# Optimization experiments

Hardware: AMD Instinct MI355X
Metric: run time of the kernel (lower is better)

Reference implementation:

```python
import jax, jax.numpy as jnp
import numpy as np

B, S, H = 1, 2048, 1024
NQ, NKV, HD = 16, 8, 64
FF, E, TOPK = 2048, 4, 2
WINDOW = 512
CAP = 50.0
CLIP_L, CLIP_R = -0.03, 1.03
EPS = 1e-5
ROPE_BASE = 10000.0


def setup_inputs() -> dict:
    key = jax.random.key(0)
    ks = jax.random.split(key, 14)
    std = 0.02
    def nrm(k, shape):
        return jax.random.normal(k, shape, jnp.float32) * std
    return {
        'x': jax.random.normal(ks[0], (B, S, H), jnp.float32),
        'norm1_w': 1.0 + nrm(ks[1], (H,)),
        'wq': nrm(ks[2], (H, NQ * HD)),
        'wk': nrm(ks[3], (H, NKV * HD)),
        'wv': nrm(ks[4], (H, NKV * HD)),
        'wo': nrm(ks[5], (NQ * HD, H)),
        'qn_w': 1.0 + nrm(ks[6], (HD,)),
        'kn_w': 1.0 + nrm(ks[7], (HD,)),
        'norm2_w': 1.0 + nrm(ks[8], (H,)),
        'gate_w': nrm(ks[9], (H, E)),
        'w_gate': nrm(ks[10], (E, H, FF)),
        'w_up': nrm(ks[11], (E, H, FF)),
        'w_down': nrm(ks[12], (E, FF, H)),
    }


def _rms(x, w):
    return x * jax.lax.rsqrt(jnp.mean(x * x, axis=-1, keepdims=True) + EPS) * w


def _rope(t):
    # t: [B, S, N, D]
    D = t.shape[-1]
    half = D // 2
    inv = 1.0 / (ROPE_BASE ** (jnp.arange(half, dtype=jnp.float32) / half))
    ang = jnp.arange(t.shape[1], dtype=jnp.float32)[:, None] * inv  # [S, half]
    cos = jnp.cos(ang)[None, :, None, :]
    sin = jnp.sin(ang)[None, :, None, :]
    t1, t2 = t[..., :half], t[..., half:]
    return jnp.concatenate([t1 * cos - t2 * sin, t1 * sin + t2 * cos], axis=-1)


def reference(x, norm1_w, wq, wk, wv, wo, qn_w, kn_w, norm2_w, gate_w, w_gate, w_up, w_down):
    # --- self-attention block ---
    xn = _rms(x, norm1_w)
    q = (xn @ wq).reshape(B, S, NQ, HD)
    k = (xn @ wk).reshape(B, S, NKV, HD)
    v = (xn @ wv).reshape(B, S, NKV, HD)
    q = _rms(_rope(q), qn_w)  # RoPE then QK-norm over head_dim
    k = _rms(_rope(k), kn_w)
    rep = NQ // NKV
    k = jnp.repeat(k, rep, axis=2)  # GQA expand to NQ heads
    v = jnp.repeat(v, rep, axis=2)
    scale = 1.0 / np.sqrt(HD).astype(np.float32)
    scores = jnp.einsum('bqhd,bkhd->bhqk', q, k) * scale
    scores = CAP * jnp.tanh(scores / CAP)  # softmax capping (overrides temperature)
    i = jnp.arange(S)[:, None]
    j = jnp.arange(S)[None, :]
    allow = (j <= i) & (i - j < WINDOW)  # causal + sliding window
    scores = jnp.where(allow[None, None], scores, -jnp.inf)
    p = jax.nn.softmax(scores, axis=-1)
    p = jnp.clip((CLIP_R - CLIP_L) * p + CLIP_L, 0.0, 1.0)  # softmax clipping
    attn = jnp.einsum('bhqk,bkhd->bqhd', p, v).reshape(B, S, NQ * HD)
    h = x + attn @ wo
    # --- MoE gated-SiLU MLP block ---
    xn2 = _rms(h, norm2_w).reshape(B * S, H)
    probs = jax.nn.softmax(xn2 @ gate_w, axis=-1)
    topv, topi = jax.lax.top_k(probs, TOPK)
    topv = topv / jnp.sum(topv, axis=-1, keepdims=True)
    T = B * S
    wdense = jnp.zeros((T, E), jnp.float32).at[jnp.arange(T)[:, None], topi].add(topv)
    g = jnp.einsum('th,ehf->etf', xn2, w_gate)
    u = jnp.einsum('th,ehf->etf', xn2, w_up)
    y = jnp.einsum('etf,efh->eth', jax.nn.silu(g) * u, w_down)
    moe = jnp.einsum('eth,te->th', y, wdense)
    return h + moe.reshape(B, S, H)
```

## Files before the change

kernel.cpp:

```cpp
#include <hip/hip_runtime.h>
#include <hip/hip_bf16.h>
#include <math.h>

#define S_LEN   2048
#define H_DIM   1024
#define N_QH    16
#define N_KVH   8
#define HEADD   64
#define FF_DIM  2048
#define N_EXP   4
#define WIN     512
#define QB      16

typedef __attribute__((ext_vector_type(8))) short bf16x8;
typedef __attribute__((ext_vector_type(4))) float f32x4;

__device__ __forceinline__ short f2bf(float x) {
  unsigned u = __float_as_uint(x);
  u += 0x7fffu + ((u >> 16) & 1u);
  return (short)(u >> 16);
}
__device__ __forceinline__ float bf2f(short h) {
  return __uint_as_float((unsigned)(unsigned short)h << 16);
}
__device__ __forceinline__ int swz(int row, int col) {
  return row * 64 + (col ^ ((row & 7) << 3));
}

__global__ __launch_bounds__(256) void k_rope_tables(float* __restrict__ ct, float* __restrict__ st) {
  int i = blockIdx.x * 256 + threadIdx.x;
  int t = i >> 5, d = i & 31;
  double inv = 1.0 / pow(10000.0, (double)d / 32.0);
  double ang = (double)t * inv;
  ct[i] = (float)cos(ang);
  st[i] = (float)sin(ang);
}

template <int MODE>
__global__ __launch_bounds__(256) void k_rmsnorm(const float* __restrict__ x,
                                                 const float* __restrict__ w,
                                                 short* __restrict__ yh,
                                                 short* __restrict__ yl,
                                                 const float* __restrict__ gw,
                                                 float* __restrict__ wd) {
  int row = blockIdx.x;
  const float4 v = ((const float4*)(x + (long)row * H_DIM))[threadIdx.x];
  float ss = v.x * v.x + v.y * v.y + v.z * v.z + v.w * v.w;
  for (int off = 32; off; off >>= 1) ss += __shfl_xor(ss, off);
  __shared__ float red[4];
  if ((threadIdx.x & 63) == 0) red[threadIdx.x >> 6] = ss;
  __syncthreads();
  ss = red[0] + red[1] + red[2] + red[3];
  float r = (float)(1.0 / sqrt((double)ss * (1.0 / 1024.0) + 1e-5));
  const float4 wv = ((const float4*)w)[threadIdx.x];
  float4 o;
  o.x = v.x * r * wv.x; o.y = v.y * r * wv.y; o.z = v.z * r * wv.z; o.w = v.w * r * wv.w;
  if (MODE == 2) {
    short h0 = f2bf(o.x), h1 = f2bf(o.y), h2 = f2bf(o.z), h3 = f2bf(o.w);
    short l0 = f2bf(o.x - bf2f(h0)), l1 = f2bf(o.y - bf2f(h1));
    short l2 = f2bf(o.z - bf2f(h2)), l3 = f2bf(o.w - bf2f(h3));
    uint2 hv = make_uint2((unsigned short)h0 | ((unsigned)(unsigned short)h1 << 16),
                          (unsigned short)h2 | ((unsigned)(unsigned short)h3 << 16));
    uint2 lv = make_uint2((unsigned short)l0 | ((unsigned)(unsigned short)l1 << 16),
                          (unsigned short)l2 | ((unsigned)(unsigned short)l3 << 16));
    ((uint2*)(yh + (long)row * H_DIM))[threadIdx.x] = hv;
    ((uint2*)(yl + (long)row * H_DIM))[threadIdx.x] = lv;
  }
  if (MODE == 3) {
    unsigned lo = (unsigned short)f2bf(o.x) | ((unsigned)(unsigned short)f2bf(o.y) << 16);
    unsigned hi = (unsigned short)f2bf(o.z) | ((unsigned)(unsigned short)f2bf(o.w) << 16);
    ((uint2*)(yh + (long)row * H_DIM))[threadIdx.x] = make_uint2(lo, hi);
    int i0 = threadIdx.x * 4;
    float4 g0 = *(const float4*)&gw[(i0 + 0) * 4];
    float4 g1 = *(const float4*)&gw[(i0 + 1) * 4];
    float4 g2 = *(const float4*)&gw[(i0 + 2) * 4];
    float4 g3 = *(const float4*)&gw[(i0 + 3) * 4];
    float p0 = o.x * g0.x + o.y * g1.x + o.z * g2.x + o.w * g3.x;
    float p1 = o.x * g0.y + o.y * g1.y + o.z * g2.y + o.w * g3.y;
    float p2 = o.x * g0.z + o.y * g1.z + o.z * g2.z + o.w * g3.z;
    float p3 = o.x * g0.w + o.y * g1.w + o.z * g2.w + o.w * g3.w;
    for (int off = 32; off; off >>= 1) {
      p0 += __shfl_xor(p0, off); p1 += __shfl_xor(p1, off);
      p2 += __shfl_xor(p2, off); p3 += __shfl_xor(p3, off);
    }
    __shared__ float gred[4][4];
    int wid = threadIdx.x >> 6;
    if ((threadIdx.x & 63) == 0) { gred[wid][0] = p0; gred[wid][1] = p1; gred[wid][2] = p2; gred[wid][3] = p3; }
    __syncthreads();
    if (threadIdx.x == 0) {
      float l[4];
      for (int e = 0; e < 4; ++e) l[e] = gred[0][e] + gred[1][e] + gred[2][e] + gred[3][e];
      int i1 = 0;
      for (int e = 1; e < 4; ++e) if (l[e] > l[i1]) i1 = e;
      int i2 = -1;
      for (int e = 0; e < 4; ++e) { if (e == i1) continue; if (i2 < 0 || l[e] > l[i2]) i2 = e; }
      float e2 = expf(l[i2] - l[i1]);
      float w1 = 1.f / (1.f + e2);
      float ov[4] = {0.f, 0.f, 0.f, 0.f};
      ov[i1] = w1; ov[i2] = 1.f - w1;
      wd[row * 4 + 0] = ov[0]; wd[row * 4 + 1] = ov[1];
      wd[row * 4 + 2] = ov[2]; wd[row * 4 + 3] = ov[3];
    }
  }
}

__global__ __launch_bounds__(256) void k_tsplit(const float* __restrict__ in,
                                                short* __restrict__ oh,
                                                short* __restrict__ ol, int R, int C) {
  __shared__ float tile[32][33];
  int bx = blockIdx.x, by = blockIdx.y;
  int lx = threadIdx.x & 31, ly = threadIdx.x >> 5;
  int xc = bx * 32 + lx;
#pragma unroll
  for (int k = 0; k < 4; ++k) {
    int y = by * 32 + ly + k * 8;
    tile[ly + k * 8][lx] = in[(long)y * C + xc];
  }
  __syncthreads();
  int ox = by * 32 + lx;
#pragma unroll
  for (int k = 0; k < 4; ++k) {
    int oy = bx * 32 + ly + k * 8;
    float v = tile[lx][ly + k * 8];
    short hb = f2bf(v);
    short lb = f2bf(v - bf2f(hb));
    oh[(long)oy * R + ox] = hb;
    ol[(long)oy * R + ox] = lb;
  }
}

__global__ __launch_bounds__(256) void k_transpose_cast(const float* __restrict__ in,
                                                        short* __restrict__ out,
                                                        int R, int C) {
  __shared__ float tile[32][33];
  int bx = blockIdx.x, by = blockIdx.y;
  int lx = threadIdx.x & 31, ly = threadIdx.x >> 5;
  int x = bx * 32 + lx;
#pragma unroll
  for (int k = 0; k < 4; ++k) {
    int y = by * 32 + ly + k * 8;
    tile[ly + k * 8][lx] = in[(long)y * C + x];
  }
  __syncthreads();
  int ox = by * 32 + lx;
#pragma unroll
  for (int k = 0; k < 4; ++k) {
    int oy = bx * 32 + ly + k * 8;
    out[(long)oy * R + ox] = f2bf(tile[lx][ly + k * 8]);
  }
}

template <int ADD>
__global__ __launch_bounds__(256) void k_gemm_split(const short* __restrict__ Ah,
                                                    const short* __restrict__ Al,
                                                    const short* __restrict__ Bh,
                                                    const short* __restrict__ Bl,
                                                    const float* __restrict__ R,
                                                    float* __restrict__ C,
                                                    int K, int ldA, int ldB, int ldC) {
  __shared__ short AsH[128 * 64], AsL[128 * 64], BsH[128 * 64], BsL[128 * 64];
  const int r0 = blockIdx.x * 128, c0 = blockIdx.y * 128;
  const int tid = threadIdx.x;
  const int wid = tid >> 6, lane = tid & 63;
  const int wr = wid >> 1, wc = wid & 1;
  const int lr = lane & 15, lg = lane >> 4;
  f32x4 zero = {0.f, 0.f, 0.f, 0.f};
  f32x4 acc[4][4];
#pragma unroll
  for (int m = 0; m < 4; ++m)
#pragma unroll
    for (int n = 0; n < 4; ++n) acc[m][n] = zero;
  for (int k0 = 0; k0 < K; k0 += 64) {
#pragma unroll
    for (int it = 0; it < 4; ++it) {
      int flat = tid + it * 256;
      int row = flat >> 3, cb = (flat & 7) * 8;
      int d = swz(row, cb);
      *(uint4*)&AsH[d] = *(const uint4*)&Ah[(long)(r0 + row) * ldA + k0 + cb];
      *(uint4*)&AsL[d] = *(const uint4*)&Al[(long)(r0 + row) * ldA + k0 + cb];
      *(uint4*)&BsH[d] = *(const uint4*)&Bh[(long)(c0 + row) * ldB + k0 + cb];
      *(uint4*)&BsL[d] = *(const uint4*)&Bl[(long)(c0 + row) * ldB + k0 + cb];
    }
    __syncthreads();
#pragma unroll
    for (int kk = 0; kk < 64; kk += 32) {
      bf16x8 ah[4], al[4], bh[4], bl[4];
#pragma unroll
      for (int m = 0; m < 4; ++m) {
        int d = swz(wr * 64 + m * 16 + lr, kk + lg * 8);
        ah[m] = *(const bf16x8*)&AsH[d];
        al[m] = *(const bf16x8*)&AsL[d];
      }
#pragma unroll
      for (int n = 0; n < 4; ++n) {
        int d = swz(wc * 64 + n * 16 + lr, kk + lg * 8);
        bh[n] = *(const bf16x8*)&BsH[d];
        bl[n] = *(const bf16x8*)&BsL[d];
      }
#pragma unroll
      for (int m = 0; m < 4; ++m)
#pragma unroll
        for (int n = 0; n < 4; ++n) {
          acc[m][n] = __builtin_amdgcn_mfma_f32_16x16x32_bf16(ah[m], bh[n], acc[m][n], 0, 0, 0);
          acc[m][n] = __builtin_amdgcn_mfma_f32_16x16x32_bf16(ah[m], bl[n], acc[m][n], 0, 0, 0);
          acc[m][n] = __builtin_amdgcn_mfma_f32_16x16x32_bf16(al[m], bh[n], acc[m][n], 0, 0, 0);
        }
    }
    __syncthreads();
  }
#pragma unroll
  for (int m = 0; m < 4; ++m)
#pragma unroll
    for (int n = 0; n < 4; ++n) {
      int col = c0 + wc * 64 + n * 16 + lr;
#pragma unroll
      for (int r = 0; r < 4; ++r) {
        int row = r0 + wr * 64 + m * 16 + lg * 4 + r;
        float v = acc[m][n][r];
        if (ADD) v += R[(long)row * ldC + col];
        C[(long)row * ldC + col] = v;
      }
    }
}

__global__ __launch_bounds__(256) void k_rope_rms(float* __restrict__ qkv,
                                                  const float* __restrict__ qn_w,
                                                  const float* __restrict__ kn_w,
                                                  const float* __restrict__ ct,
                                                  const float* __restrict__ st) {
  int idx = blockIdx.x * 4 + (threadIdx.x >> 6);
  int lane = threadIdx.x & 63;
  int t = idx / 24, hh = idx - t * 24;
  long base; const float* w;
  if (hh < N_QH) { base = (long)t * 2048 + hh * HEADD;              w = qn_w; }
  else           { base = (long)t * 2048 + 1024 + (hh - N_QH) * HEADD; w = kn_w; }
  float x = qkv[base + lane];
  float partner = __shfl_xor(x, 32);
  int d = lane & 31;
  float cs = ct[t * 32 + d], sn = st[t * 32 + d];
  float r = x * cs + partner * ((lane < 32) ? -sn : sn);
  float ss = r * r;
  for (int off = 32; off; off >>= 1) ss += __shfl_xor(ss, off);
  float rr = (float)(1.0 / sqrt((double)ss * (1.0 / 64.0) + 1e-5));
  qkv[base + lane] = r * rr * w[lane];
}

__global__ __launch_bounds__(256) void k_attn_mfma(const float* __restrict__ qkv,
                                                   short* __restrict__ attHi,
                                                   short* __restrict__ attLo) {
  __shared__ short Kh[64][72], Kl[64][72];
  __shared__ float sc[QB][580];
  __shared__ float row_a[QB];
  const int i0 = blockIdx.x * QB;
  const int hq = blockIdx.y;
  const int kvh = hq >> 1;
  const int tid = threadIdx.x;
  const int wv = tid >> 6, lane = tid & 63;
  const int lr = lane & 15, lg = lane >> 4;
  const int jstart = max(0, i0 - (WIN - 1));
  const int nch = (i0 + QB - jstart + 63) >> 6;
  const int ncols = nch * 64;
  f32x4 zero = {0.f, 0.f, 0.f, 0.f};

  bf16x8 qh[2], ql[2];
  {
    const float* qp = &qkv[(long)(i0 + lr) * 2048 + hq * HEADD];
#pragma unroll
    for (int kk = 0; kk < 2; ++kk) {
      float4 f0 = *(const float4*)&qp[kk * 32 + lg * 8];
      float4 f1 = *(const float4*)&qp[kk * 32 + lg * 8 + 4];
      float ff[8] = {f0.x, f0.y, f0.z, f0.w, f1.x, f1.y, f1.z, f1.w};
      bf16x8 h, l;
#pragma unroll
      for (int u = 0; u < 8; ++u) {
        short hb = f2bf(ff[u]);
        h[u] = hb; l[u] = f2bf(ff[u] - bf2f(hb));
      }
      qh[kk] = h; ql[kk] = l;
    }
  }

  for (int ch = 0; ch < nch; ++ch) {
    int jb = jstart + ch * 64;
    {
      int key = tid >> 2, dbase = (tid & 3) * 16;
      int j = jb + key;
      const float* kp = &qkv[(long)j * 2048 + 1024 + kvh * HEADD];
#pragma unroll
      for (int q4 = 0; q4 < 4; ++q4) {
        int d = dbase + q4 * 4;
        float4 f = make_float4(0.f, 0.f, 0.f, 0.f);
        if (j < S_LEN) f = *(const float4*)&kp[d];
        short h0 = f2bf(f.x), h1 = f2bf(f.y), h2 = f2bf(f.z), h3 = f2bf(f.w);
        short l0 = f2bf(f.x - bf2f(h0)), l1 = f2bf(f.y - bf2f(h1));
        short l2 = f2bf(f.z - bf2f(h2)), l3 = f2bf(f.w - bf2f(h3));
        *(uint2*)&Kh[key][d] = make_uint2(
            (unsigned short)h0 | ((unsigned)(unsigned short)h1 << 16),
            (unsigned short)h2 | ((unsigned)(unsigned short)h3 << 16));
        *(uint2*)&Kl[key][d] = make_uint2(
            (unsigned short)l0 | ((unsigned)(unsigned short)l1 << 16),
            (unsigned short)l2 | ((unsigned)(unsigned short)l3 << 16));
      }
    }
    __syncthreads();
    f32x4 s = zero;
#pragma unroll
    for (int kk = 0; kk < 2; ++kk) {
      bf16x8 kh = *(const bf16x8*)&Kh[wv * 16 + lr][kk * 32 + lg * 8];
      bf16x8 kl = *(const bf16x8*)&Kl[wv * 16 + lr][kk * 32 + lg * 8];
      s = __builtin_amdgcn_mfma_f32_16x16x32_bf16(qh[kk], kh, s, 0, 0, 0);
      s = __builtin_amdgcn_mfma_f32_16x16x32_bf16(qh[kk], kl, s, 0, 0, 0);
      s = __builtin_amdgcn_mfma_f32_16x16x32_bf16(ql[kk], kh, s, 0, 0, 0);
    }
    int colbase = ch * 64 + wv * 16;
#pragma unroll
    for (int r = 0; r < 4; ++r) {
      int q = 4 * lg + r;
      int i = i0 + q;
      int j = jb + wv * 16 + lr;
      float v = s[r] * 0.125f;
      v = 50.f * tanhf(v * 0.02f);
      bool allow = (j <= i) && (i - j < WIN);
      sc[q][colbase + lr] = allow ? v : -1e30f;
    }
    __syncthreads();
  }

  for (int r = wv * 4; r < wv * 4 + 4; ++r) {
    float mx = -1e30f;
    for (int n = lane; n < ncols; n += 64) mx = fmaxf(mx, sc[r][n]);
    for (int off = 32; off; off >>= 1) mx = fmaxf(mx, __shfl_xor(mx, off));
    float sum = 0.f;
    for (int n = lane; n < ncols; n += 64) {
      float p = expf(sc[r][n] - mx);
      sc[r][n] = p; sum += p;
    }
    for (int off = 32; off; off >>= 1) sum += __shfl_xor(sum, off);
    if (lane == 0) row_a[r] = 1.06f / sum;
  }
  __syncthreads();

  {
    int q = tid >> 4;
    float a = row_a[q];
    for (int n = (tid & 15); n < ncols; n += 16) {
      float e = sc[q][n];
      float p = fminf(fmaxf(fmaf(a, e, -0.03f), 0.f), 1.f);
      short ph = f2bf(p);
      short pl = f2bf(p - bf2f(ph));
      *(unsigned*)&sc[q][n] =
          (unsigned)(unsigned short)ph | ((unsigned)(unsigned short)pl << 16);
    }
  }
  __syncthreads();

  f32x4 oacc = zero;
  for (int ch = 0; ch < nch; ++ch) {
    int jb = jstart + ch * 64;
    {
      int j = jb + (lane);
      int dbase = wv * 16;
      bool ok = (j < S_LEN);
      const float* vp = &qkv[(long)j * 2048 + 1536 + kvh * HEADD];
#pragma unroll
      for (int dd = 0; dd < 16; ++dd) {
        float f = ok ? vp[dbase + dd] : 0.f;
        short hb = f2bf(f);
        Kh[dbase + dd][lane] = hb;
        Kl[dbase + dd][lane] = f2bf(f - bf2f(hb));
      }
    }
    __syncthreads();
#pragma unroll
    for (int kk = 0; kk < 2; ++kk) {
      const unsigned* pp = (const unsigned*)&sc[lr][ch * 64 + kk * 32 + lg * 8];
      uint4 w0 = *(const uint4*)&pp[0];
      uint4 w1 = *(const uint4*)&pp[4];
      bf16x8 pa, pb;
      pa[0] = (short)w0.x; pb[0] = (short)(w0.x >> 16);
      pa[1] = (short)w0.y; pb[1] = (short)(w0.y >> 16);
      pa[2] = (short)w0.z; pb[2] = (short)(w0.z >> 16);
      pa[3] = (short)w0.w; pb[3] = (short)(w0.w >> 16);
      pa[4] = (short)w1.x; pb[4] = (short)(w1.x >> 16);
      pa[5] = (short)w1.y; pb[5] = (short)(w1.y >> 16);
      pa[6] = (short)w1.z; pb[6] = (short)(w1.z >> 16);
      pa[7] = (short)w1.w; pb[7] = (short)(w1.w >> 16);
      bf16x8 vh = *(const bf16x8*)&Kh[wv * 16 + lr][kk * 32 + lg * 8];
      bf16x8 vl = *(const bf16x8*)&Kl[wv * 16 + lr][kk * 32 + lg * 8];
      oacc = __builtin_amdgcn_mfma_f32_16x16x32_bf16(pa, vh, oacc, 0, 0, 0);
      oacc = __builtin_amdgcn_mfma_f32_16x16x32_bf16(pa, vl, oacc, 0, 0, 0);
      oacc = __builtin_amdgcn_mfma_f32_16x16x32_bf16(pb, vh, oacc, 0, 0, 0);
    }
    __syncthreads();
  }
#pragma unroll
  for (int r = 0; r < 4; ++r) {
    int q = 4 * lg + r;
    int d = wv * 16 + lr;
    long ob = (long)(i0 + q) * 1024 + hq * HEADD + d;
    float v = oacc[r];
    short hb = f2bf(v);
    attHi[ob] = hb;
    attLo[ob] = f2bf(v - bf2f(hb));
  }
}

template <int ATOMIC>
__global__ __launch_bounds__(256) void k_gemm_bf16(const short* __restrict__ A,
                                                   const short* __restrict__ Bt,
                                                   float* __restrict__ C,
                                                   int K, int ldA, int ldB, int ldC,
                                                   long sA, long sB, long sC) {
  __shared__ short As[128 * 64];
  __shared__ short Bs[128 * 64];
  const int e = blockIdx.z;
  A += (long)e * sA; Bt += (long)e * sB; C += (long)e * sC;
  const int r0 = blockIdx.x * 128, c0 = blockIdx.y * 128;
  const int tid = threadIdx.x;
  const int wid = tid >> 6, lane = tid & 63;
  const int wr = wid >> 1, wc = wid & 1;
  const int lr = lane & 15, lg = lane >> 4;
  f32x4 zero = {0.f, 0.f, 0.f, 0.f};
  f32x4 acc[4][4];
#pragma unroll
  for (int m = 0; m < 4; ++m)
#pragma unroll
    for (int n = 0; n < 4; ++n) acc[m][n] = zero;
  for (int k0 = 0; k0 < K; k0 += 64) {
#pragma unroll
    for (int it = 0; it < 4; ++it) {
      int flat = tid + it * 256;
      int row = flat >> 3, cb = (flat & 7) * 8;
      int d = swz(row, cb);
      *(uint4*)&As[d] = *(const uint4*)&A[(long)(r0 + row) * ldA + k0 + cb];
      *(uint4*)&Bs[d] = *(const uint4*)&Bt[(long)(c0 + row) * ldB + k0 + cb];
    }
    __syncthreads();
#pragma unroll
    for (int kk = 0; kk < 64; kk += 32) {
      bf16x8 af[4], bfr[4];
#pragma unroll
      for (int m = 0; m < 4; ++m) af[m] = *(const bf16x8*)&As[swz(wr * 64 + m * 16 + lr, kk + lg * 8)];
#pragma unroll
      for (int n = 0; n < 4; ++n) bfr[n] = *(const bf16x8*)&Bs[swz(wc * 64 + n * 16 + lr, kk + lg * 8)];
#pragma unroll
      for (int m = 0; m < 4; ++m)
#pragma unroll
        for (int n = 0; n < 4; ++n)
          acc[m][n] = __builtin_amdgcn_mfma_f32_16x16x32_bf16(af[m], bfr[n], acc[m][n], 0, 0, 0);
    }
    __syncthreads();
  }
#pragma unroll
  for (int m = 0; m < 4; ++m)
#pragma unroll
    for (int n = 0; n < 4; ++n) {
      int col = c0 + wc * 64 + n * 16 + lr;
#pragma unroll
      for (int r = 0; r < 4; ++r) {
        int row = r0 + wr * 64 + m * 16 + lg * 4 + r;
        float v = acc[m][n][r];
        if (ATOMIC) atomicAdd(&C[(long)row * ldC + col], v);
        else        C[(long)row * ldC + col] = v;
      }
    }
}

__global__ __launch_bounds__(256) void k_moe_act(const float* __restrict__ gu,
                                                 const float* __restrict__ wd,
                                                 short* __restrict__ aAll,
                                                 int e) {
  long i4 = (long)blockIdx.x * 256 + threadIdx.x;
  int t  = (int)(i4 >> 9);
  int f4 = (int)(i4 & 511);
  float wte = wd[t * 4 + e];
  float4 g = ((const float4*)gu)[(long)t * 1024 + f4];
  float4 u = ((const float4*)gu)[(long)t * 1024 + 512 + f4];
  float4 s;
  s.x = wte * u.x * g.x / (1.f + expf(-g.x));
  s.y = wte * u.y * g.y / (1.f + expf(-g.y));
  s.z = wte * u.z * g.z / (1.f + expf(-g.z));
  s.w = wte * u.w * g.w / (1.f + expf(-g.w));
  unsigned lo = (unsigned short)f2bf(s.x) | ((unsigned)(unsigned short)f2bf(s.y) << 16);
  unsigned hi = (unsigned short)f2bf(s.z) | ((unsigned)(unsigned short)f2bf(s.w) << 16);
  ((uint2*)(aAll + ((long)e << 22)))[i4] = make_uint2(lo, hi);
}

extern "C" void kernel_launch(void* const* d_in, const int* in_sizes, int n_in,
                              void* d_out, int out_size, void* d_ws, size_t ws_size,
                              hipStream_t stream) {
  const float* x       = (const float*)d_in[0];
  const float* norm1_w = (const float*)d_in[1];
  const float* wq      = (const float*)d_in[2];
  const float* wk      = (const float*)d_in[3];
  const float* wv      = (const float*)d_in[4];
  const float* wo      = (const float*)d_in[5];
  const float* qn_w    = (const float*)d_in[6];
  const float* kn_w    = (const float*)d_in[7];
  const float* norm2_w = (const float*)d_in[8];
  const float* gate_w  = (const float*)d_in[9];
  const float* w_gate  = (const float*)d_in[10];
  const float* w_up    = (const float*)d_in[11];
  const float* w_down  = (const float*)d_in[12];
  float* out = (float*)d_out;
  char* ws = (char*)d_ws;
  const unsigned long MB = 1ul << 20;

  float* ropeC = (float*)(ws + 0);
  float* ropeS = (float*)(ws + 256 * 1024);
  float* qkv   = (float*)(ws + 1 * MB);
  short* xnHi  = (short*)(ws + 17 * MB);
  short* xnLo  = (short*)(ws + 21 * MB);
  short* attHi = (short*)(ws + 25 * MB);
  short* attLo = (short*)(ws + 29 * MB);
  float* gu    = (float*)(ws + 1 * MB);
  short* qkvWh = (short*)(ws + 33 * MB);
  short* qkvWl = (short*)(ws + 37 * MB);
  short* woTh  = (short*)(ws + 41 * MB);
  short* woTl  = (short*)(ws + 43 * MB);
  float* h     = (float*)(ws + 45 * MB);
  short* guT   = (short*)(ws + 45 * MB);
  short* x2b   = (short*)(ws + 53 * MB);
  float* wd    = (float*)(ws + 57 * MB);
  short* dT    = (short*)(ws + 58 * MB);
  short* aAll  = (short*)(ws + 74 * MB);

  k_rope_tables<<<256, 256, 0, stream>>>(ropeC, ropeS);
  k_rmsnorm<2><<<S_LEN, 256, 0, stream>>>(x, norm1_w, xnHi, xnLo, nullptr, nullptr);
  k_tsplit<<<dim3(32, 32), 256, 0, stream>>>(wq, qkvWh, qkvWl, 1024, 1024);
  k_tsplit<<<dim3(16, 32), 256, 0, stream>>>(wk, qkvWh + 1024 * 1024, qkvWl + 1024 * 1024, 1024, 512);
  k_tsplit<<<dim3(16, 32), 256, 0, stream>>>(wv, qkvWh + 1536 * 1024, qkvWl + 1536 * 1024, 1024, 512);
  k_tsplit<<<dim3(32, 32), 256, 0, stream>>>(wo, woTh, woTl, 1024, 1024);
  k_gemm_split<0><<<dim3(16, 16), 256, 0, stream>>>(xnHi, xnLo, qkvWh, qkvWl, nullptr, qkv,
                                                    1024, 1024, 1024, 2048);
  k_rope_rms<<<(S_LEN * 24) / 4, 256, 0, stream>>>(qkv, qn_w, kn_w, ropeC, ropeS);
  k_attn_mfma<<<dim3(S_LEN / QB, N_QH), 256, 0, stream>>>(qkv, attHi, attLo);
  k_gemm_split<1><<<dim3(16, 8), 256, 0, stream>>>(attHi, attLo, woTh, woTl, x, h,
                                                   1024, 1024, 1024, 1024);
  k_rmsnorm<3><<<S_LEN, 256, 0, stream>>>(h, norm2_w, x2b, nullptr, gate_w, wd);
  hipMemcpyAsync(out, h, (size_t)S_LEN * H_DIM * sizeof(float), hipMemcpyDeviceToDevice, stream);
  for (int e = 0; e < N_EXP; ++e)
    k_transpose_cast<<<dim3(1024 / 32, 2048 / 32), 256, 0, stream>>>(
        w_down + (long)e * FF_DIM * H_DIM, dT + (long)e * H_DIM * FF_DIM, 2048, 1024);
  for (int e = 0; e < N_EXP; ++e) {
    k_transpose_cast<<<dim3(2048 / 32, 1024 / 32), 256, 0, stream>>>(
        w_gate + (long)e * H_DIM * FF_DIM, guT, 1024, 2048);
    k_transpose_cast<<<dim3(2048 / 32, 1024 / 32), 256, 0, stream>>>(
        w_up + (long)e * H_DIM * FF_DIM, guT + (long)FF_DIM * H_DIM, 1024, 2048);
    k_gemm_bf16<0><<<dim3(16, 32), 256, 0, stream>>>(x2b, guT, gu, 1024, 1024, 1024, 4096, 0, 0, 0);
    k_moe_act<<<4096, 256, 0, stream>>>(gu, wd, aAll, e);
  }
  k_gemm_bf16<1><<<dim3(16, 8, N_EXP), 256, 0, stream>>>(
      aAll, dT, out, 2048, 2048, 2048, 1024,
      (long)S_LEN * FF_DIM, (long)H_DIM * FF_DIM, 0);
}
```

Baseline: 719.6 us.

## Precompute split-bf16 K and transposed V once, read directly in attention

Adds a kernel that converts K to hi/lo bf16 and V to transposed hi/lo bf16 once per KV head. Previously every attention block redid this conversion per chunk through shared memory. The attention kernel now loads MFMA operands straight from global memory and drops the per-chunk barriers. It also aligns the window start to 64 keys. The cost is an extra launch, extra workspace traffic, and uncoalesced per-lane global loads in place of LDS reads.

```diff
diff --git a/kernel.cpp b/kernel.cpp
--- a/kernel.cpp
+++ b/kernel.cpp
@@ -11,6 +11,7 @@
 #define N_EXP   4
 #define WIN     512
 #define QB      16
+#define SCS     596
 
 typedef __attribute__((ext_vector_type(8))) short bf16x8;
 typedef __attribute__((ext_vector_type(4))) float f32x4;
@@ -22,6 +23,9 @@
 }
 __device__ __forceinline__ float bf2f(short h) {
   return __uint_as_float((unsigned)(unsigned short)h << 16);
+}
+__device__ __forceinline__ unsigned pk2(short a, short b) {
+  return (unsigned)(unsigned short)a | ((unsigned)(unsigned short)b << 16);
 }
 __device__ __forceinline__ int swz(int row, int col) {
   return row * 64 + (col ^ ((row & 7) << 3));
@@ -59,17 +63,12 @@
     short h0 = f2bf(o.x), h1 = f2bf(o.y), h2 = f2bf(o.z), h3 = f2bf(o.w);
     short l0 = f2bf(o.x - bf2f(h0)), l1 = f2bf(o.y - bf2f(h1));
     short l2 = f2bf(o.z - bf2f(h2)), l3 = f2bf(o.w - bf2f(h3));
-    uint2 hv = make_uint2((unsigned short)h0 | ((unsigned)(unsigned short)h1 << 16),
-                          (unsigned short)h2 | ((unsigned)(unsigned short)h3 << 16));
-    uint2 lv = make_uint2((unsigned short)l0 | ((unsigned)(unsigned short)l1 << 16),
-                          (unsigned short)l2 | ((unsigned)(unsigned short)l3 << 16));
-    ((uint2*)(yh + (long)row * H_DIM))[threadIdx.x] = hv;
-    ((uint2*)(yl + (long)row * H_DIM))[threadIdx.x] = lv;
+    ((uint2*)(yh + (long)row * H_DIM))[threadIdx.x] = make_uint2(pk2(h0, h1), pk2(h2, h3));
+    ((uint2*)(yl + (long)row * H_DIM))[threadIdx.x] = make_uint2(pk2(l0, l1), pk2(l2, l3));
   }
   if (MODE == 3) {
-    unsigned lo = (unsigned short)f2bf(o.x) | ((unsigned)(unsigned short)f2bf(o.y) << 16);
-    unsigned hi = (unsigned short)f2bf(o.z) | ((unsigned)(unsigned short)f2bf(o.w) << 16);
-    ((uint2*)(yh + (long)row * H_DIM))[threadIdx.x] = make_uint2(lo, hi);
+    ((uint2*)(yh + (long)row * H_DIM))[threadIdx.x] =
+        make_uint2(pk2(f2bf(o.x), f2bf(o.y)), pk2(f2bf(o.z), f2bf(o.w)));
     int i0 = threadIdx.x * 4;
     float4 g0 = *(const float4*)&gw[(i0 + 0) * 4];
     float4 g1 = *(const float4*)&gw[(i0 + 1) * 4];
@@ -245,11 +244,59 @@
   qkv[base + lane] = r * rr * w[lane];
 }
 
-__global__ __launch_bounds__(256) void k_attn_mfma(const float* __restrict__ qkv,
-                                                   short* __restrict__ attHi,
-                                                   short* __restrict__ attLo) {
-  __shared__ short Kh[64][72], Kl[64][72];
-  __shared__ float sc[QB][580];
+__global__ __launch_bounds__(256) void k_kv_split(const float* __restrict__ qkv,
+                                                  short* __restrict__ Kbh, short* __restrict__ Kbl,
+                                                  short* __restrict__ Vth, short* __restrict__ Vtl) {
+  const int kvh = blockIdx.y;
+  const int jb = blockIdx.x * 64;
+  const int tid = threadIdx.x;
+  {
+    int j = jb + (tid >> 2);
+    int dq = (tid & 3) * 16;
+    const float* kp = &qkv[(long)j * 2048 + 1024 + kvh * HEADD + dq];
+    long ob = ((long)kvh * S_LEN + j) * HEADD + dq;
+#pragma unroll
+    for (int u4 = 0; u4 < 4; ++u4) {
+      float4 f = *(const float4*)&kp[u4 * 4];
+      short h0 = f2bf(f.x), h1 = f2bf(f.y), h2 = f2bf(f.z), h3 = f2bf(f.w);
+      short l0 = f2bf(f.x - bf2f(h0)), l1 = f2bf(f.y - bf2f(h1));
+      short l2 = f2bf(f.z - bf2f(h2)), l3 = f2bf(f.w - bf2f(h3));
+      *(uint2*)&Kbh[ob + u4 * 4] = make_uint2(pk2(h0, h1), pk2(h2, h3));
+      *(uint2*)&Kbl[ob + u4 * 4] = make_uint2(pk2(l0, l1), pk2(l2, l3));
+    }
+  }
+  {
+    int d = tid & 63;
+    int j0 = jb + (tid >> 6) * 16;
+    short hb[16], lb[16];
+#pragma unroll
+    for (int u = 0; u < 16; ++u) {
+      float f = qkv[(long)(j0 + u) * 2048 + 1536 + kvh * HEADD + d];
+      hb[u] = f2bf(f);
+      lb[u] = f2bf(f - bf2f(hb[u]));
+    }
+    long ob = ((long)kvh * HEADD + d) * S_LEN + j0;
+#pragma unroll
+    for (int w = 0; w < 2; ++w) {
+      uint4 oh, ol;
+      oh.x = pk2(hb[w * 8 + 0], hb[w * 8 + 1]); oh.y = pk2(hb[w * 8 + 2], hb[w * 8 + 3]);
+      oh.z = pk2(hb[w * 8 + 4], hb[w * 8 + 5]); oh.w = pk2(hb[w * 8 + 6], hb[w * 8 + 7]);
+      ol.x = pk2(lb[w * 8 + 0], lb[w * 8 + 1]); ol.y = pk2(lb[w * 8 + 2], lb[w * 8 + 3]);
+      ol.z = pk2(lb[w * 8 + 4], lb[w * 8 + 5]); ol.w = pk2(lb[w * 8 + 6], lb[w * 8 + 7]);
+      *(uint4*)&Vth[ob + w * 8] = oh;
+      *(uint4*)&Vtl[ob + w * 8] = ol;
+    }
+  }
+}
+
+__global__ __launch_bounds__(256) void k_attn2(const float* __restrict__ qkv,
+                                               const short* __restrict__ Kbh,
+                                               const short* __restrict__ Kbl,
+                                               const short* __restrict__ Vth,
+                                               const short* __restrict__ Vtl,
+                                               short* __restrict__ attHi,
+                                               short* __restrict__ attLo) {
+  __shared__ float sc[QB][SCS];
   __shared__ float row_a[QB];
   const int i0 = blockIdx.x * QB;
   const int hq = blockIdx.y;
@@ -257,10 +304,14 @@
   const int tid = threadIdx.x;
   const int wv = tid >> 6, lane = tid & 63;
   const int lr = lane & 15, lg = lane >> 4;
-  const int jstart = max(0, i0 - (WIN - 1));
+  const int jstart = (i0 >= WIN) ? ((i0 - (WIN - 1)) & ~63) : 0;
   const int nch = (i0 + QB - jstart + 63) >> 6;
   const int ncols = nch * 64;
   f32x4 zero = {0.f, 0.f, 0.f, 0.f};
+  const short* Kh_p = Kbh + (long)kvh * S_LEN * HEADD;
+  const short* Kl_p = Kbl + (long)kvh * S_LEN * HEADD;
+  const short* Vh_p = Vth + (long)kvh * HEADD * S_LEN;
+  const short* Vl_p = Vtl + (long)kvh * HEADD * S_LEN;
 
   bf16x8 qh[2], ql[2];
   {
@@ -282,49 +333,29 @@
 
   for (int ch = 0; ch < nch; ++ch) {
     int jb = jstart + ch * 64;
-    {
-      int key = tid >> 2, dbase = (tid & 3) * 16;
-      int j = jb + key;
-      const float* kp = &qkv[(long)j * 2048 + 1024 + kvh * HEADD];
-#pragma unroll
-      for (int q4 = 0; q4 < 4; ++q4) {
-        int d = dbase + q4 * 4;
-        float4 f = make_float4(0.f, 0.f, 0.f, 0.f);
-        if (j < S_LEN) f = *(const float4*)&kp[d];
-        short h0 = f2bf(f.x), h1 = f2bf(f.y), h2 = f2bf(f.z), h3 = f2bf(f.w);
-        short l0 = f2bf(f.x - bf2f(h0)), l1 = f2bf(f.y - bf2f(h1));
-        short l2 = f2bf(f.z - bf2f(h2)), l3 = f2bf(f.w - bf2f(h3));
-        *(uint2*)&Kh[key][d] = make_uint2(
-            (unsigned short)h0 | ((unsigned)(unsigned short)h1 << 16),
-            (unsigned short)h2 | ((unsigned)(unsigned short)h3 << 16));
-        *(uint2*)&Kl[key][d] = make_uint2(
-            (unsigned short)l0 | ((unsigned)(unsigned short)l1 << 16),
-            (unsigned short)l2 | ((unsigned)(unsigned short)l3 << 16));
-      }
-    }
-    __syncthreads();
+    int jrow = jb + wv * 16 + lr;
+    int jc = min(jrow, S_LEN - 1);
     f32x4 s = zero;
 #pragma unroll
     for (int kk = 0; kk < 2; ++kk) {
-      bf16x8 kh = *(const bf16x8*)&Kh[wv * 16 + lr][kk * 32 + lg * 8];
-      bf16x8 kl = *(const bf16x8*)&Kl[wv * 16 + lr][kk * 32 + lg * 8];
+      bf16x8 kh = *(const bf16x8*)&Kh_p[(long)jc * HEADD + kk * 32 + lg * 8];
+      bf16x8 kl = *(const bf16x8*)&Kl_p[(long)jc * HEADD + kk * 32 + lg * 8];
       s = __builtin_amdgcn_mfma_f32_16x16x32_bf16(qh[kk], kh, s, 0, 0, 0);
       s = __builtin_amdgcn_mfma_f32_16x16x32_bf16(qh[kk], kl, s, 0, 0, 0);
       s = __builtin_amdgcn_mfma_f32_16x16x32_bf16(ql[kk], kh, s, 0, 0, 0);
     }
-    int colbase = ch * 64 + wv * 16;
+    int col = ch * 64 + wv * 16 + lr;
 #pragma unroll
     for (int r = 0; r < 4; ++r) {
       int q = 4 * lg + r;
       int i = i0 + q;
-      int j = jb + wv * 16 + lr;
       float v = s[r] * 0.125f;
       v = 50.f * tanhf(v * 0.02f);
-      bool allow = (j <= i) && (i - j < WIN);
-      sc[q][colbase + lr] = allow ? v : -1e30f;
-    }
-    __syncthreads();
-  }
+      bool allow = (jrow <= i) && (i - jrow < WIN);
+      sc[q][col] = allow ? v : -1e30f;
+    }
+  }
+  __syncthreads();
 
   for (int r = wv * 4; r < wv * 4 + 4; ++r) {
     float mx = -1e30f;
@@ -348,8 +379,7 @@
       float p = fminf(fmaxf(fmaf(a, e, -0.03f), 0.f), 1.f);
       short ph = f2bf(p);
       short pl = f2bf(p - bf2f(ph));
-      *(unsigned*)&sc[q][n] =
-          (unsigned)(unsigned short)ph | ((unsigned)(unsigned short)pl << 16);
+      *(unsigned*)&sc[q][n] = pk2(ph, pl);
     }
   }
   __syncthreads();
@@ -357,22 +387,10 @@
   f32x4 oacc = zero;
   for (int ch = 0; ch < nch; ++ch) {
     int jb = jstart + ch * 64;
-    {
-      int j = jb + (lane);
-      int dbase = wv * 16;
-      bool ok = (j < S_LEN);
-      const float* vp = &qkv[(long)j * 2048 + 1536 + kvh * HEADD];
-#pragma unroll
-      for (int dd = 0; dd < 16; ++dd) {
-        float f = ok ? vp[dbase + dd] : 0.f;
-        short hb = f2bf(f);
-        Kh[dbase + dd][lane] = hb;
-        Kl[dbase + dd][lane] = f2bf(f - bf2f(hb));
-      }
-    }
-    __syncthreads();
 #pragma unroll
     for (int kk = 0; kk < 2; ++kk) {
+      int js = jb + kk * 32 + lg * 8;
+      int jcb = min(js, S_LEN - 8);
       const unsigned* pp = (const unsigned*)&sc[lr][ch * 64 + kk * 32 + lg * 8];
       uint4 w0 = *(const uint4*)&pp[0];
       uint4 w1 = *(const uint4*)&pp[4];
@@ -385,13 +403,12 @@
       pa[5] = (short)w1.y; pb[5] = (short)(w1.y >> 16);
       pa[6] = (short)w1.z; pb[6] = (short)(w1.z >> 16);
       pa[7] = (short)w1.w; pb[7] = (short)(w1.w >> 16);
-      bf16x8 vh = *(const bf16x8*)&Kh[wv * 16 + lr][kk * 32 + lg * 8];
-      bf16x8 vl = *(const bf16x8*)&Kl[wv * 16 + lr][kk * 32 + lg * 8];
+      bf16x8 vh = *(const bf16x8*)&Vh_p[(long)(wv * 16 + lr) * S_LEN + jcb];
+      bf16x8 vl = *(const bf16x8*)&Vl_p[(long)(wv * 16 + lr) * S_LEN + jcb];
       oacc = __builtin_amdgcn_mfma_f32_16x16x32_bf16(pa, vh, oacc, 0, 0, 0);
       oacc = __builtin_amdgcn_mfma_f32_16x16x32_bf16(pa, vl, oacc, 0, 0, 0);
       oacc = __builtin_amdgcn_mfma_f32_16x16x32_bf16(pb, vh, oacc, 0, 0, 0);
     }
-    __syncthreads();
   }
 #pragma unroll
   for (int r = 0; r < 4; ++r) {
@@ -481,9 +498,8 @@
   s.y = wte * u.y * g.y / (1.f + expf(-g.y));
   s.z = wte * u.z * g.z / (1.f + expf(-g.z));
   s.w = wte * u.w * g.w / (1.f + expf(-g.w));
-  unsigned lo = (unsigned short)f2bf(s.x) | ((unsigned)(unsigned short)f2bf(s.y) << 16);
-  unsigned hi = (unsigned short)f2bf(s.z) | ((unsigned)(unsigned short)f2bf(s.w) << 16);
-  ((uint2*)(aAll + ((long)e << 22)))[i4] = make_uint2(lo, hi);
+  ((uint2*)(aAll + ((long)e << 22)))[i4] =
+      make_uint2(pk2(f2bf(s.x), f2bf(s.y)), pk2(f2bf(s.z), f2bf(s.w)));
 }
 
 extern "C" void kernel_launch(void* const* d_in, const int* in_sizes, int n_in,
@@ -523,6 +539,10 @@
   short* x2b   = (short*)(ws + 53 * MB);
   float* wd    = (float*)(ws + 57 * MB);
   short* dT    = (short*)(ws + 58 * MB);
+  short* Kbh   = (short*)(ws + 58 * MB);
+  short* Kbl   = (short*)(ws + 60 * MB);
+  short* Vth   = (short*)(ws + 62 * MB);
+  short* Vtl   = (short*)(ws + 64 * MB);
   short* aAll  = (short*)(ws + 74 * MB);
 
   k_rope_tables<<<256, 256, 0, stream>>>(ropeC, ropeS);
@@ -534,7 +554,8 @@
   k_gemm_split<0><<<dim3(16, 16), 256, 0, stream>>>(xnHi, xnLo, qkvWh, qkvWl, nullptr, qkv,
                                                     1024, 1024, 1024, 2048);
   k_rope_rms<<<(S_LEN * 24) / 4, 256, 0, stream>>>(qkv, qn_w, kn_w, ropeC, ropeS);
-  k_attn_mfma<<<dim3(S_LEN / QB, N_QH), 256, 0, stream>>>(qkv, attHi, attLo);
+  k_kv_split<<<dim3(S_LEN / 64, N_KVH), 256, 0, stream>>>(qkv, Kbh, Kbl, Vth, Vtl);
+  k_attn2<<<dim3(S_LEN / QB, N_QH), 256, 0, stream>>>(qkv, Kbh, Kbl, Vth, Vtl, attHi, attLo);
   k_gemm_split<1><<<dim3(16, 8), 256, 0, stream>>>(attHi, attLo, woTh, woTl, x, h,
                                                    1024, 1024, 1024, 1024);
   k_rmsnorm<3><<<S_LEN, 256, 0, stream>>>(h, norm2_w, x2b, nullptr, gate_w, wd);
```

Result: faster. 579.7 us (-19.4%).
